# Optimization experiments

Measured on AMD Instinct MI355X. Metric: run time of the kernel, lower is better.

The kernel has to match this reference:

```python
import jax, jax.numpy as jnp
import numpy as np

T, B, NC, NM, H = 256, 2048, 3, 125, 256  # time, batch, classes, measures, hidden
IN = NC + NM


def setup_inputs() -> dict:
    key = jax.random.key(0)
    ks = jax.random.split(key, 12)
    seq = jax.random.normal(ks[0], (T, B, IN), jnp.float32)
    nan_mask = jax.random.uniform(ks[1], (T, B, IN)) < 0.1
    nan_mask = nan_mask.at[0].set(False)  # first step must be observed
    seq = jnp.where(nan_mask, jnp.nan, seq)
    s = 1.0 / np.sqrt(H)
    u = lambda k, shp: jax.random.uniform(k, shp, jnp.float32, -s, s)
    return {
        "pair_seq": seq,
        "W_ih": u(ks[2], (4 * H, IN)),
        "W_hh": u(ks[3], (4 * H, H)),
        "b_ih": u(ks[4], (4 * H,)),
        "b_hh": u(ks[5], (4 * H,)),
        "W_cat": u(ks[6], (NC, H)),
        "b_cat": u(ks[7], (NC,)),
        "W_val": u(ks[8], (NM, H)),
        "b_val": u(ks[9], (NM,)),
    }


def reference(pair_seq, W_ih, W_hh, b_ih, b_hh, W_cat, b_cat, W_val, b_val):
    cat_seq = pair_seq[:, :, :NC]
    val_seq = pair_seq[:, :, NC:]
    bsz = pair_seq.shape[1]
    h0 = jnp.zeros((bsz, H), pair_seq.dtype)
    c0 = jnp.zeros((bsz, H), pair_seq.dtype)
    # eval mode: dropout masks are all-ones, so they are identity multiplies

    def lstm_cell(x, h, c):
        gates = x @ W_ih.T + b_ih + h @ W_hh.T + b_hh  # [B, 4H]
        i, f, g, o = jnp.split(gates, 4, axis=-1)
        c2 = jax.nn.sigmoid(f) * c + jax.nn.sigmoid(i) * jnp.tanh(g)
        h2 = jax.nn.sigmoid(o) * jnp.tanh(c2)
        return h2, c2

    def step(carry, nxt):
        h, c, i_cat, i_val = carry
        cat_next, val_next = nxt
        x = jnp.concatenate([i_cat, i_val], axis=-1)
        h, c = lstm_cell(x, h, c)
        o_cat = jax.nn.softmax(h @ W_cat.T + b_cat, axis=-1)
        o_val = h @ W_val.T + b_val + i_val
        # impute NaNs in the next timestep with (detached) predictions
        i_cat2 = jnp.where(jnp.isnan(cat_next), jax.lax.stop_gradient(o_cat), cat_next)
        i_val2 = jnp.where(jnp.isnan(val_next), jax.lax.stop_gradient(o_val), val_next)
        return (h, c, i_cat2, i_val2), (o_cat, o_val)

    init = (h0, c0, cat_seq[0], val_seq[0])
    _, (out_cat, out_val) = jax.lax.scan(step, init, (cat_seq[1:], val_seq[1:]))
    return jnp.concatenate([out_cat, out_val], axis=2)  # [T-1, B, NC+NM]
```

## Files before the change

### kernel.cpp

```cpp
#include <hip/hip_runtime.h>
#include <hip/hip_bf16.h>

constexpr int TSTEPS = 255;
constexpr int XROW   = 392;

typedef __attribute__((ext_vector_type(8))) short short8;
typedef __attribute__((ext_vector_type(4))) float f32x4;
typedef __attribute__((ext_vector_type(16))) float f32x16;
typedef __attribute__((ext_vector_type(4))) int i32x4;
typedef __attribute__((ext_vector_type(2))) unsigned int u32x2;

__device__ __forceinline__ unsigned short f2bf(float f) {
    __hip_bfloat16 h = __float2bfloat16(f);
    return *reinterpret_cast<unsigned short*>(&h);
}
__device__ __forceinline__ float bf2f(unsigned short u) {
    __hip_bfloat16 h;
    *reinterpret_cast<unsigned short*>(&h) = u;
    return __bfloat162float(h);
}
__device__ __forceinline__ float sigf(float x) {
    return __builtin_amdgcn_rcpf(1.f + __expf(-x));
}
__device__ __forceinline__ float tanh_fast(float x) {
    x = fminf(fmaxf(x, -15.f), 15.f);
    float e = __expf(-2.f * x);
    return (1.f - e) * __builtin_amdgcn_rcpf(1.f + e);
}

__device__ __forceinline__ i32x4 load_coh16(const void* p) {
    i32x4 r;
    asm volatile("global_load_dwordx4 %0, %1, off sc0 sc1" : "=v"(r) : "v"(p) : "memory");
    return r;
}
__device__ __forceinline__ void store_coh16(void* p, i32x4 v) {
    asm volatile("global_store_dwordx4 %0, %1, off sc0 sc1" :: "v"(p), "v"(v) : "memory");
}

__device__ __forceinline__ void groupbar(unsigned int* cnt, unsigned int tgt, int tid) {
    asm volatile("s_waitcnt vmcnt(0)" ::: "memory");
    __syncthreads();
    if (tid == 0) {
        __hip_atomic_fetch_add(cnt, 1u, __ATOMIC_RELAXED, __HIP_MEMORY_SCOPE_AGENT);
        while (__hip_atomic_load(cnt, __ATOMIC_RELAXED, __HIP_MEMORY_SCOPE_AGENT) < tgt)
            __builtin_amdgcn_s_sleep(1);
    }
    __syncthreads();
}

__global__ void prep_kernel(const float* __restrict__ Wih, const float* __restrict__ Whh,
                            const float* __restrict__ bih, const float* __restrict__ bhh,
                            const float* __restrict__ Wcat, const float* __restrict__ bcat,
                            const float* __restrict__ Wval, const float* __restrict__ bval,
                            unsigned short* __restrict__ Wg, unsigned short* __restrict__ Wo,
                            float* __restrict__ bg, float* __restrict__ bo,
                            unsigned int* __restrict__ flags) {
    int idx = blockIdx.x * 256 + threadIdx.x;
    if (idx < 393216) {
        int j   = idx & 7;
        int l   = (idx >> 3) & 63;
        int t24 = idx >> 9;
        int kt  = t24 % 24;
        int u   = t24 / 24;
        int gm = u & 3, ss = u >> 2;
        int pm = l & 31;
        int n  = (pm & 3) * 256 + ss * 32 + gm * 8 + (pm >> 2);
        int k  = kt * 16 + (l >> 5) * 8 + j;
        float v = (k < 128) ? Wih[n * 128 + k] : Whh[n * 256 + (k - 128)];
        Wg[idx] = f2bf(v);
    } else if (idx < 425984) {
        int i2 = idx - 393216;
        int j = i2 & 7, ll = (i2 >> 3) & 63, kt = (i2 >> 9) & 15, om = i2 >> 13;
        int n = om * 32 + (ll & 31);
        int k = kt * 16 + (ll >> 5) * 8 + j;
        float v = (n < 3) ? Wcat[n * 256 + k] : Wval[(n - 3) * 256 + k];
        Wo[i2] = f2bf(v);
    } else if (idx < 427008) {
        int i3 = idx - 425984;
        bg[i3] = bih[i3] + bhh[i3];
    } else if (idx < 427136) {
        int i4 = idx - 427008;
        bo[i4] = (i4 < 3) ? bcat[i4] : bval[i4 - 3];
    } else if (idx < 428160) {
        flags[idx - 427136] = 0u;
    }
}

__global__ __launch_bounds__(512, 2) void rnn_kernel(
    const float* __restrict__ seq,
    const unsigned short* __restrict__ Wg, const unsigned short* __restrict__ Wo,
    const float* __restrict__ bg, const float* __restrict__ bo,
    unsigned short* __restrict__ hb, unsigned int* __restrict__ flags,
    float* __restrict__ out) {

    __shared__ __align__(16) unsigned short xh[64][XROW];
    __shared__ __align__(16) float bgl[128];
    __shared__ __align__(16) float obl[128];
    extern __shared__ char lds_pad[];
    (void)lds_pad;

    const int tid = threadIdx.x;
    const int wv  = tid >> 6, l = tid & 63;
    const int c   = l & 31, lh = l >> 5;
    const int s   = blockIdx.x >> 5;
    const int r   = blockIdx.x & 31;
    const int row0 = r * 64;
    const int hm  = wv >> 1;
    const int bn  = wv & 1;
    const int R   = bn * 32 + c;

    unsigned int* cnt = flags + r * 16;

    short8 wga[24], woa[16];
    {
        const short8* WgV = reinterpret_cast<const short8*>(Wg);
        const short8* WoV = reinterpret_cast<const short8*>(Wo);
#pragma unroll
        for (int kt = 0; kt < 24; ++kt) wga[kt] = WgV[(size_t)(((s * 4 + hm) * 24 + kt) * 64) + l];
#pragma unroll
        for (int kt = 0; kt < 16; ++kt) woa[kt] = WoV[(size_t)((hm * 16 + kt) * 64) + l];
    }

    if (tid < 128) {
        int gm_ = tid >> 5, lh_ = (tid >> 4) & 1, i_ = tid & 15;
        int pm = (i_ & 3) + 8 * (i_ >> 2) + 4 * lh_;
        bgl[tid] = bg[(pm & 3) * 256 + s * 32 + gm_ * 8 + (pm >> 2)];
        obl[tid] = bo[gm_ * 32 + 8 * (i_ >> 2) + 4 * lh_ + (i_ & 3)];
    }

#pragma unroll
    for (int i = 0; i < 4; ++i) {
        int ch = i * 512 + tid;
        int row = ch >> 5, c4 = ch & 31;
        f32x4 v = *reinterpret_cast<const f32x4*>(seq + (size_t)(row0 + row) * 128 + c4 * 4);
        unsigned short* p = &xh[row][c4 * 4];
        p[0] = f2bf(v[0]); p[1] = f2bf(v[1]); p[2] = f2bf(v[2]); p[3] = f2bf(v[3]);
    }
    {
        short8 z = {0, 0, 0, 0, 0, 0, 0, 0};
#pragma unroll
        for (int i = 0; i < 4; ++i) {
            int ch = i * 512 + tid;
            int row = ch >> 5, k8 = ch & 31;
            *reinterpret_cast<short8*>(&xh[row][128 + k8 * 8]) = z;
        }
    }

    unsigned int xv[8];
    {
        const float* sp0 = seq + (size_t)(row0 + R) * 128 + hm * 32 + 4 * lh;
#pragma unroll
        for (int g = 0; g < 4; ++g) {
            f32x4 v = *reinterpret_cast<const f32x4*>(sp0 + 8 * g);
            xv[2 * g]     = (unsigned int)f2bf(v[0]) | ((unsigned int)f2bf(v[1]) << 16);
            xv[2 * g + 1] = (unsigned int)f2bf(v[2]) | ((unsigned int)f2bf(v[3]) << 16);
        }
    }

    float cst[4] = {0.f, 0.f, 0.f, 0.f};
    const float* bgp = &bgl[(hm * 2 + lh) * 16];
    const float* obp = &obl[(hm * 2 + lh) * 16];
    const unsigned short* xrow = &xh[R][0];

    __syncthreads();

    for (int t = 0; t < TSTEPS; ++t) {
        f32x4 sq[4];
        if (t < TSTEPS - 1) {
            const float* sp = seq + ((size_t)(t + 1) * 2048 + row0 + R) * 128 + hm * 32 + 4 * lh;
#pragma unroll
            for (int g = 0; g < 4; ++g) sq[g] = *reinterpret_cast<const f32x4*>(sp + 8 * g);
        }

        f32x16 acc;
#pragma unroll
        for (int i = 0; i < 16; ++i) acc[i] = bgp[i];
#pragma unroll
        for (int kt = 0; kt < 24; ++kt) {
            short8 b = *reinterpret_cast<const short8*>(xrow + kt * 16 + lh * 8);
            acc = __builtin_amdgcn_mfma_f32_32x32x16_bf16(wga[kt], b, acc, 0, 0, 0);
        }

        float hn[4];
#pragma unroll
        for (int g = 0; g < 4; ++g) {
            float cn = sigf(acc[4 * g + 1]) * cst[g] + sigf(acc[4 * g]) * tanh_fast(acc[4 * g + 2]);
            hn[g] = sigf(acc[4 * g + 3]) * tanh_fast(cn);
            cst[g] = cn;
        }
        {
            i32x4 hw;
#pragma unroll
            for (int g = 0; g < 4; ++g) {
                float other = __shfl_xor(hn[g], 32);
                unsigned short lo = f2bf(lh ? other : hn[g]);
                unsigned short hi = f2bf(lh ? hn[g] : other);
                hw[g] = (int)((unsigned int)lo | ((unsigned int)hi << 16));
            }
            if (lh == 0) {
                char* hp = (char*)hb + (size_t)(t & 1) * 1048576 + (size_t)r * 32768
                         + (size_t)R * 512 + s * 64 + hm * 16;
                store_coh16(hp, hw);
            }
        }

        groupbar(cnt, 8u * (t + 1), tid);

        {
            const unsigned short* hsrc = hb + (size_t)(t & 1) * 524288 + (size_t)r * 16384;
            i32x4 hv[4];
#pragma unroll
            for (int i = 0; i < 4; ++i) {
                int ch = i * 512 + tid;
                hv[i] = load_coh16(hsrc + (size_t)((ch >> 5) * 256 + (ch & 31) * 8));
            }
            asm volatile("s_waitcnt vmcnt(0)" ::: "memory");
            __builtin_amdgcn_sched_barrier(0);
#pragma unroll
            for (int i = 0; i < 4; ++i) {
                int ch = i * 512 + tid;
                *reinterpret_cast<i32x4*>(&xh[ch >> 5][128 + (ch & 31) * 8]) = hv[i];
            }
        }
        __syncthreads();

        f32x16 acc2;
#pragma unroll
        for (int i = 0; i < 16; ++i) acc2[i] = obp[i];
#pragma unroll
        for (int kt = 0; kt < 16; ++kt) {
            short8 b = *reinterpret_cast<const short8*>(xrow + 128 + kt * 16 + lh * 8);
            acc2 = __builtin_amdgcn_mfma_f32_32x32x16_bf16(woa[kt], b, acc2, 0, 0, 0);
        }

        float vv[16];
#pragma unroll
        for (int g = 0; g < 4; ++g) {
#pragma unroll
            for (int j = 0; j < 4; ++j) {
                int i = 4 * g + j;
                float v = acc2[i];
                unsigned short x16 = (unsigned short)(xv[2 * g + (j >> 1)] >> ((j & 1) * 16));
                bool isCat = (g == 0) && (j < 3) && ((hm | lh) == 0);
                if (!isCat) v += bf2f(x16);
                vv[i] = v;
            }
        }
        if ((hm | lh) == 0) {
            float mx = fmaxf(fmaxf(vv[0], vv[1]), vv[2]);
            float e0 = __expf(vv[0] - mx), e1 = __expf(vv[1] - mx), e2 = __expf(vv[2] - mx);
            float rs = __builtin_amdgcn_rcpf(e0 + e1 + e2);
            vv[0] = e0 * rs; vv[1] = e1 * rs; vv[2] = e2 * rs;
        }

        if (hm == (s >> 1)) {
            int gp = (s & 1) * 2;
            size_t ob0 = ((size_t)t * 2048 + row0 + R) * 128 + hm * 32 + 4 * lh;
            f32x4 o0 = {vv[4 * gp], vv[4 * gp + 1], vv[4 * gp + 2], vv[4 * gp + 3]};
            f32x4 o1 = {vv[4 * gp + 4], vv[4 * gp + 5], vv[4 * gp + 6], vv[4 * gp + 7]};
            *reinterpret_cast<f32x4*>(out + ob0 + 8 * gp) = o0;
            *reinterpret_cast<f32x4*>(out + ob0 + 8 * gp + 8) = o1;
        }
        if (t < TSTEPS - 1) {
#pragma unroll
            for (int g = 0; g < 4; ++g) {
                unsigned int w0 = 0, w1 = 0;
#pragma unroll
                for (int j = 0; j < 4; ++j) {
                    unsigned short s16 = f2bf(sq[g][j]);
                    bool nan = (s16 & 0x7fff) > 0x7f80;
                    unsigned short nv = nan ? f2bf(vv[4 * g + j]) : s16;
                    if (j < 2) w0 |= (unsigned int)nv << (16 * j);
                    else       w1 |= (unsigned int)nv << (16 * (j - 2));
                }
                xv[2 * g] = w0; xv[2 * g + 1] = w1;
                u32x2 wp = {w0, w1};
                *reinterpret_cast<u32x2*>(&xh[R][hm * 32 + 8 * g + 4 * lh]) = wp;
            }
        }
        __syncthreads();
    }
}

extern "C" void kernel_launch(void* const* d_in, const int* in_sizes, int n_in,
                              void* d_out, int out_size, void* d_ws, size_t ws_size,
                              hipStream_t stream) {
    const float* seq  = (const float*)d_in[0];
    const float* Wih  = (const float*)d_in[1];
    const float* Whh  = (const float*)d_in[2];
    const float* bih  = (const float*)d_in[3];
    const float* bhh  = (const float*)d_in[4];
    const float* Wcat = (const float*)d_in[5];
    const float* bcat = (const float*)d_in[6];
    const float* Wval = (const float*)d_in[7];
    const float* bval = (const float*)d_in[8];

    char* ws = (char*)d_ws;
    unsigned short* Wg    = (unsigned short*)(ws);
    unsigned short* Wo    = (unsigned short*)(ws + 786432);
    float*          bgp   = (float*)(ws + 851968);
    float*          bop   = (float*)(ws + 856064);
    unsigned int*   flags = (unsigned int*)(ws + 856576);
    unsigned short* hbuf  = (unsigned short*)(ws + 860672);

    prep_kernel<<<1673, 256, 0, stream>>>(Wih, Whh, bih, bhh, Wcat, bcat, Wval, bval,
                                          Wg, Wo, bgp, bop, flags);
    rnn_kernel<<<256, 512, 32768, stream>>>(seq, Wg, Wo, bgp, bop, hbuf, flags, (float*)d_out);
}
```

Baseline: 1.123 ms.

## Specialize waves into gate and output roles with ping-pong batch halves

Splits each block's eight waves into four gate waves and four output waves, and splits the block's 64 batch rows into two halves processed in alternating slots. In each slot, gate waves compute the LSTM step for one half while output waves wait for the other half's h, load it, compute predictions and impute the next input. The block-wide group barrier is replaced by per-half arrival counters that only the consuming waves spin on. The gate and output MFMA chains are split into two independent accumulators, and s_setprio is raised around them. The goal is to hide cross-block h exchange latency behind matrix work. The cost is more synchronisation points per step and only half the waves doing MFMA in any slot.

New measurement: 1.378 ms. 22.7% more time.

```diff
diff --git a/kernel.cpp b/kernel.cpp
--- a/kernel.cpp
+++ b/kernel.cpp
@@ -35,17 +35,6 @@
 }
 __device__ __forceinline__ void store_coh16(void* p, i32x4 v) {
     asm volatile("global_store_dwordx4 %0, %1, off sc0 sc1" :: "v"(p), "v"(v) : "memory");
-}
-
-__device__ __forceinline__ void groupbar(unsigned int* cnt, unsigned int tgt, int tid) {
-    asm volatile("s_waitcnt vmcnt(0)" ::: "memory");
-    __syncthreads();
-    if (tid == 0) {
-        __hip_atomic_fetch_add(cnt, 1u, __ATOMIC_RELAXED, __HIP_MEMORY_SCOPE_AGENT);
-        while (__hip_atomic_load(cnt, __ATOMIC_RELAXED, __HIP_MEMORY_SCOPE_AGENT) < tgt)
-            __builtin_amdgcn_s_sleep(1);
-    }
-    __syncthreads();
 }
 
 __global__ void prep_kernel(const float* __restrict__ Wih, const float* __restrict__ Whh,
@@ -86,6 +75,133 @@
     }
 }
 
+#define SLOT(PA, TG, TO, CSTA, XVB) do {                                            \
+    constexpr int PB_ = (PA) ^ 1;                                                   \
+    const int tg_ = (TG), to_ = (TO);                                               \
+    const bool gact = isGW && (tg_ < TSTEPS);                                       \
+    const bool oact = (!isGW) && (to_ >= 0);                                        \
+    f32x16 acc, accB;                                                               \
+    f32x4 sq[4];                                                                    \
+              \
+    if (gact) {                                                                     \
+        const unsigned short* xrow = &xh[(PA) * 32 + c][0];                         \
+        _Pragma("unroll") for (int i = 0; i < 16; ++i) { acc[i] = breg[i]; accB[i] = 0.f; } \
+        __builtin_amdgcn_s_setprio(1);                                              \
+        _Pragma("unroll") for (int kt = 0; kt < 24; kt += 2) {                      \
+            short8 b0 = *reinterpret_cast<const short8*>(xrow + kt * 16 + lh * 8);  \
+            short8 b1 = *reinterpret_cast<const short8*>(xrow + (kt + 1) * 16 + lh * 8); \
+            acc  = __builtin_amdgcn_mfma_f32_32x32x16_bf16(wreg[kt], b0, acc, 0, 0, 0); \
+            accB = __builtin_amdgcn_mfma_f32_32x32x16_bf16(wreg[kt + 1], b1, accB, 0, 0, 0); \
+        }                                                                           \
+        __builtin_amdgcn_s_setprio(0);                                              \
+        _Pragma("unroll") for (int i = 0; i < 16; ++i) acc[i] += accB[i];           \
+    } else if (oact) {                                                              \
+        if (to_ + 1 < TSTEPS) {                                                     \
+            const float* sp = seq + ((size_t)(to_ + 1) * 2048 + row0 + PB_ * 32 + c) * 128 \
+                            + hm * 32 + 4 * lh;                                     \
+            _Pragma("unroll") for (int g = 0; g < 4; ++g)                           \
+                sq[g] = *reinterpret_cast<const f32x4*>(sp + 8 * g);                \
+        }                                                                           \
+        unsigned int tgt = 32u * (unsigned)(to_ + 1);                               \
+        while (__hip_atomic_load(cntP[PB_], __ATOMIC_RELAXED, __HIP_MEMORY_SCOPE_AGENT) < tgt) \
+            __builtin_amdgcn_s_sleep(1);                                            \
+        asm volatile("" ::: "memory");                                              \
+        {                                                                           \
+            const unsigned short* hsrc = hb + (size_t)(to_ & 1) * 524288 + (size_t)r * 16384; \
+            int tid2 = tid & 255;                                                   \
+            i32x4 hv[4];                                                            \
+            _Pragma("unroll") for (int i2 = 0; i2 < 4; ++i2) {                      \
+                int ch = i2 * 256 + tid2;                                           \
+                hv[i2] = load_coh16(hsrc + (size_t)((PB_ * 32 + (ch >> 5)) * 256 + (ch & 31) * 8)); \
+            }                                                                       \
+            asm volatile("s_waitcnt vmcnt(0)" ::: "memory");                        \
+            __builtin_amdgcn_sched_barrier(0);                                      \
+            _Pragma("unroll") for (int i2 = 0; i2 < 4; ++i2) {                      \
+                int ch = i2 * 256 + tid2;                                           \
+                *reinterpret_cast<i32x4*>(&xh[PB_ * 32 + (ch >> 5)][128 + (ch & 31) * 8]) = hv[i2]; \
+            }                                                                       \
+        }                                                                           \
+    }                                                                               \
+    __syncthreads();                \
+       \
+    if (gact) {                                                                     \
+        float hn[4];                                                                \
+        _Pragma("unroll") for (int g = 0; g < 4; ++g) {                             \
+            float cn = sigf(acc[4 * g + 1]) * CSTA[g]                               \
+                     + sigf(acc[4 * g + 0]) * tanh_fast(acc[4 * g + 2]);            \
+            hn[g] = sigf(acc[4 * g + 3]) * tanh_fast(cn);                           \
+            CSTA[g] = cn;                                                           \
+        }                                                                           \
+        i32x4 hw;                                                                   \
+        _Pragma("unroll") for (int g = 0; g < 4; ++g) {                             \
+            float other = __shfl_xor(hn[g], 32);                                    \
+            unsigned short lo = f2bf(lh ? other : hn[g]);                           \
+            unsigned short hi = f2bf(lh ? hn[g] : other);                           \
+            hw[g] = (int)((unsigned)lo | ((unsigned)hi << 16));                     \
+        }                                                                           \
+        if (lh == 0) {                                                              \
+            char* hp = (char*)hb + (size_t)(tg_ & 1) * 1048576 + (size_t)r * 32768  \
+                     + (size_t)((PA) * 32 + c) * 512 + s * 64 + hm * 16;            \
+            store_coh16(hp, hw);                                                    \
+        }                                                                           \
+        asm volatile("s_waitcnt vmcnt(0)" ::: "memory");                            \
+        if (l == 0)                                                                 \
+            __hip_atomic_fetch_add(cntP[PA], 1u, __ATOMIC_RELAXED, __HIP_MEMORY_SCOPE_AGENT); \
+    } else if (oact) {                                                              \
+        const unsigned short* xrow = &xh[PB_ * 32 + c][0];                          \
+        _Pragma("unroll") for (int i = 0; i < 16; ++i) { acc[i] = breg[i]; accB[i] = 0.f; } \
+        __builtin_amdgcn_s_setprio(1);                                              \
+        _Pragma("unroll") for (int kt = 0; kt < 16; kt += 2) {                      \
+            short8 b0 = *reinterpret_cast<const short8*>(xrow + 128 + kt * 16 + lh * 8); \
+            short8 b1 = *reinterpret_cast<const short8*>(xrow + 128 + (kt + 1) * 16 + lh * 8); \
+            acc  = __builtin_amdgcn_mfma_f32_32x32x16_bf16(wreg[kt], b0, acc, 0, 0, 0); \
+            accB = __builtin_amdgcn_mfma_f32_32x32x16_bf16(wreg[kt + 1], b1, accB, 0, 0, 0); \
+        }                                                                           \
+        __builtin_amdgcn_s_setprio(0);                                              \
+        float vv[16];                                                               \
+        _Pragma("unroll") for (int g = 0; g < 4; ++g) {                             \
+            _Pragma("unroll") for (int j = 0; j < 4; ++j) {                         \
+                int i = 4 * g + j;                                                  \
+                float v = acc[i] + accB[i];                                         \
+                unsigned short x16 = (unsigned short)(XVB[2 * g + (j >> 1)] >> ((j & 1) * 16)); \
+                bool isCat = (g == 0) && (j < 3) && hm0lh0;                         \
+                if (!isCat) v += bf2f(x16);                                         \
+                vv[i] = v;                                                          \
+            }                                                                       \
+        }                                                                           \
+        if (hm0lh0) {                                                               \
+            float mx = fmaxf(fmaxf(vv[0], vv[1]), vv[2]);                           \
+            float e0 = __expf(vv[0] - mx), e1 = __expf(vv[1] - mx), e2 = __expf(vv[2] - mx); \
+            float rs = __builtin_amdgcn_rcpf(e0 + e1 + e2);                         \
+            vv[0] = e0 * rs; vv[1] = e1 * rs; vv[2] = e2 * rs;                      \
+        }                                                                           \
+        if (hm == (s >> 1)) {                                                       \
+            int gp = (s & 1) * 2;                                                   \
+            size_t ob0 = ((size_t)to_ * 2048 + row0 + PB_ * 32 + c) * 128 + hm * 32 + 4 * lh; \
+            f32x4 o0 = {vv[4 * gp], vv[4 * gp + 1], vv[4 * gp + 2], vv[4 * gp + 3]}; \
+            f32x4 o1 = {vv[4 * gp + 4], vv[4 * gp + 5], vv[4 * gp + 6], vv[4 * gp + 7]}; \
+            *reinterpret_cast<f32x4*>(out + ob0 + 8 * gp) = o0;                     \
+            *reinterpret_cast<f32x4*>(out + ob0 + 8 * gp + 8) = o1;                 \
+        }                                                                           \
+        if (to_ < TSTEPS - 1) {                                                     \
+            _Pragma("unroll") for (int g = 0; g < 4; ++g) {                         \
+                unsigned int w0 = 0, w1 = 0;                                        \
+                _Pragma("unroll") for (int j = 0; j < 4; ++j) {                     \
+                    float sqv = sq[g][j];                                           \
+                    float xf = (sqv != sqv) ? vv[4 * g + j] : sqv;                  \
+                    unsigned short nv = f2bf(xf);                                   \
+                    if (j < 2) w0 |= (unsigned)nv << (16 * j);                      \
+                    else       w1 |= (unsigned)nv << (16 * (j - 2));                \
+                }                                                                   \
+                XVB[2 * g] = w0; XVB[2 * g + 1] = w1;                               \
+                u32x2 wp = {w0, w1};                                                \
+                *reinterpret_cast<u32x2*>(&xh[PB_ * 32 + c][hm * 32 + 8 * g + 4 * lh]) = wp; \
+            }                                                                       \
+        }                                                                           \
+    }                                                                               \
+    __syncthreads();                                                  \
+} while (0)
+
 __global__ __launch_bounds__(512, 2) void rnn_kernel(
     const float* __restrict__ seq,
     const unsigned short* __restrict__ Wg, const unsigned short* __restrict__ Wo,
@@ -105,20 +221,23 @@
     const int s   = blockIdx.x >> 5;
     const int r   = blockIdx.x & 31;
     const int row0 = r * 64;
-    const int hm  = wv >> 1;
-    const int bn  = wv & 1;
-    const int R   = bn * 32 + c;
-
-    unsigned int* cnt = flags + r * 16;
-
-    short8 wga[24], woa[16];
-    {
+    const bool isGW = wv < 4;
+    const int hm  = wv & 3;
+    const bool hm0lh0 = (hm == 0) && (lh == 0);
+
+    unsigned int* cntP[2] = {flags + r * 32, flags + r * 32 + 16};
+
+    short8 wreg[24];
+    if (isGW) {
         const short8* WgV = reinterpret_cast<const short8*>(Wg);
+#pragma unroll
+        for (int kt = 0; kt < 24; ++kt) wreg[kt] = WgV[(size_t)(((s * 4 + hm) * 24 + kt) * 64) + l];
+    } else {
         const short8* WoV = reinterpret_cast<const short8*>(Wo);
 #pragma unroll
-        for (int kt = 0; kt < 24; ++kt) wga[kt] = WgV[(size_t)(((s * 4 + hm) * 24 + kt) * 64) + l];
-#pragma unroll
-        for (int kt = 0; kt < 16; ++kt) woa[kt] = WoV[(size_t)((hm * 16 + kt) * 64) + l];
+        for (int kt = 0; kt < 16; ++kt) wreg[kt] = WoV[(size_t)((hm * 16 + kt) * 64) + l];
+#pragma unroll
+        for (int kt = 16; kt < 24; ++kt) wreg[kt] = wreg[0];
     }
 
     if (tid < 128) {
@@ -141,145 +260,43 @@
 #pragma unroll
         for (int i = 0; i < 4; ++i) {
             int ch = i * 512 + tid;
-            int row = ch >> 5, k8 = ch & 31;
-            *reinterpret_cast<short8*>(&xh[row][128 + k8 * 8]) = z;
+            *reinterpret_cast<short8*>(&xh[ch >> 5][128 + (ch & 31) * 8]) = z;
         }
     }
 
-    unsigned int xv[8];
-    {
-        const float* sp0 = seq + (size_t)(row0 + R) * 128 + hm * 32 + 4 * lh;
+    unsigned int xv0[8], xv1[8];
+    if (!isGW) {
+        const float* sp0 = seq + (size_t)(row0 + c) * 128 + hm * 32 + 4 * lh;
 #pragma unroll
         for (int g = 0; g < 4; ++g) {
             f32x4 v = *reinterpret_cast<const f32x4*>(sp0 + 8 * g);
-            xv[2 * g]     = (unsigned int)f2bf(v[0]) | ((unsigned int)f2bf(v[1]) << 16);
-            xv[2 * g + 1] = (unsigned int)f2bf(v[2]) | ((unsigned int)f2bf(v[3]) << 16);
+            xv0[2 * g]     = (unsigned)f2bf(v[0]) | ((unsigned)f2bf(v[1]) << 16);
+            xv0[2 * g + 1] = (unsigned)f2bf(v[2]) | ((unsigned)f2bf(v[3]) << 16);
         }
-    }
-
-    float cst[4] = {0.f, 0.f, 0.f, 0.f};
-    const float* bgp = &bgl[(hm * 2 + lh) * 16];
-    const float* obp = &obl[(hm * 2 + lh) * 16];
-    const unsigned short* xrow = &xh[R][0];
+        const float* sp1 = seq + (size_t)(row0 + 32 + c) * 128 + hm * 32 + 4 * lh;
+#pragma unroll
+        for (int g = 0; g < 4; ++g) {
+            f32x4 v = *reinterpret_cast<const f32x4*>(sp1 + 8 * g);
+            xv1[2 * g]     = (unsigned)f2bf(v[0]) | ((unsigned)f2bf(v[1]) << 16);
+            xv1[2 * g + 1] = (unsigned)f2bf(v[2]) | ((unsigned)f2bf(v[3]) << 16);
+        }
+    }
+
+    float cst0[4] = {0.f, 0.f, 0.f, 0.f};
+    float cst1[4] = {0.f, 0.f, 0.f, 0.f};
 
     __syncthreads();
 
-    for (int t = 0; t < TSTEPS; ++t) {
-        f32x4 sq[4];
-        if (t < TSTEPS - 1) {
-            const float* sp = seq + ((size_t)(t + 1) * 2048 + row0 + R) * 128 + hm * 32 + 4 * lh;
-#pragma unroll
-            for (int g = 0; g < 4; ++g) sq[g] = *reinterpret_cast<const f32x4*>(sp + 8 * g);
-        }
-
-        f32x16 acc;
-#pragma unroll
-        for (int i = 0; i < 16; ++i) acc[i] = bgp[i];
-#pragma unroll
-        for (int kt = 0; kt < 24; ++kt) {
-            short8 b = *reinterpret_cast<const short8*>(xrow + kt * 16 + lh * 8);
-            acc = __builtin_amdgcn_mfma_f32_32x32x16_bf16(wga[kt], b, acc, 0, 0, 0);
-        }
-
-        float hn[4];
-#pragma unroll
-        for (int g = 0; g < 4; ++g) {
-            float cn = sigf(acc[4 * g + 1]) * cst[g] + sigf(acc[4 * g]) * tanh_fast(acc[4 * g + 2]);
-            hn[g] = sigf(acc[4 * g + 3]) * tanh_fast(cn);
-            cst[g] = cn;
-        }
-        {
-            i32x4 hw;
-#pragma unroll
-            for (int g = 0; g < 4; ++g) {
-                float other = __shfl_xor(hn[g], 32);
-                unsigned short lo = f2bf(lh ? other : hn[g]);
-                unsigned short hi = f2bf(lh ? hn[g] : other);
-                hw[g] = (int)((unsigned int)lo | ((unsigned int)hi << 16));
-            }
-            if (lh == 0) {
-                char* hp = (char*)hb + (size_t)(t & 1) * 1048576 + (size_t)r * 32768
-                         + (size_t)R * 512 + s * 64 + hm * 16;
-                store_coh16(hp, hw);
-            }
-        }
-
-        groupbar(cnt, 8u * (t + 1), tid);
-
-        {
-            const unsigned short* hsrc = hb + (size_t)(t & 1) * 524288 + (size_t)r * 16384;
-            i32x4 hv[4];
-#pragma unroll
-            for (int i = 0; i < 4; ++i) {
-                int ch = i * 512 + tid;
-                hv[i] = load_coh16(hsrc + (size_t)((ch >> 5) * 256 + (ch & 31) * 8));
-            }
-            asm volatile("s_waitcnt vmcnt(0)" ::: "memory");
-            __builtin_amdgcn_sched_barrier(0);
-#pragma unroll
-            for (int i = 0; i < 4; ++i) {
-                int ch = i * 512 + tid;
-                *reinterpret_cast<i32x4*>(&xh[ch >> 5][128 + (ch & 31) * 8]) = hv[i];
-            }
-        }
-        __syncthreads();
-
-        f32x16 acc2;
-#pragma unroll
-        for (int i = 0; i < 16; ++i) acc2[i] = obp[i];
-#pragma unroll
-        for (int kt = 0; kt < 16; ++kt) {
-            short8 b = *reinterpret_cast<const short8*>(xrow + 128 + kt * 16 + lh * 8);
-            acc2 = __builtin_amdgcn_mfma_f32_32x32x16_bf16(woa[kt], b, acc2, 0, 0, 0);
-        }
-
-        float vv[16];
-#pragma unroll
-        for (int g = 0; g < 4; ++g) {
-#pragma unroll
-            for (int j = 0; j < 4; ++j) {
-                int i = 4 * g + j;
-                float v = acc2[i];
-                unsigned short x16 = (unsigned short)(xv[2 * g + (j >> 1)] >> ((j & 1) * 16));
-                bool isCat = (g == 0) && (j < 3) && ((hm | lh) == 0);
-                if (!isCat) v += bf2f(x16);
-                vv[i] = v;
-            }
-        }
-        if ((hm | lh) == 0) {
-            float mx = fmaxf(fmaxf(vv[0], vv[1]), vv[2]);
-            float e0 = __expf(vv[0] - mx), e1 = __expf(vv[1] - mx), e2 = __expf(vv[2] - mx);
-            float rs = __builtin_amdgcn_rcpf(e0 + e1 + e2);
-            vv[0] = e0 * rs; vv[1] = e1 * rs; vv[2] = e2 * rs;
-        }
-
-        if (hm == (s >> 1)) {
-            int gp = (s & 1) * 2;
-            size_t ob0 = ((size_t)t * 2048 + row0 + R) * 128 + hm * 32 + 4 * lh;
-            f32x4 o0 = {vv[4 * gp], vv[4 * gp + 1], vv[4 * gp + 2], vv[4 * gp + 3]};
-            f32x4 o1 = {vv[4 * gp + 4], vv[4 * gp + 5], vv[4 * gp + 6], vv[4 * gp + 7]};
-            *reinterpret_cast<f32x4*>(out + ob0 + 8 * gp) = o0;
-            *reinterpret_cast<f32x4*>(out + ob0 + 8 * gp + 8) = o1;
-        }
-        if (t < TSTEPS - 1) {
-#pragma unroll
-            for (int g = 0; g < 4; ++g) {
-                unsigned int w0 = 0, w1 = 0;
-#pragma unroll
-                for (int j = 0; j < 4; ++j) {
-                    unsigned short s16 = f2bf(sq[g][j]);
-                    bool nan = (s16 & 0x7fff) > 0x7f80;
-                    unsigned short nv = nan ? f2bf(vv[4 * g + j]) : s16;
-                    if (j < 2) w0 |= (unsigned int)nv << (16 * j);
-                    else       w1 |= (unsigned int)nv << (16 * (j - 2));
-                }
-                xv[2 * g] = w0; xv[2 * g + 1] = w1;
-                u32x2 wp = {w0, w1};
-                *reinterpret_cast<u32x2*>(&xh[R][hm * 32 + 8 * g + 4 * lh]) = wp;
-            }
-        }
-        __syncthreads();
-    }
+    float breg[16];
+#pragma unroll
+    for (int i = 0; i < 16; ++i)
+        breg[i] = isGW ? bgl[(hm * 2 + lh) * 16 + i] : obl[(hm * 2 + lh) * 16 + i];
+
+    for (int tt = 0; tt < TSTEPS; ++tt) {
+        SLOT(0, tt, tt - 1, cst0, xv1);
+        SLOT(1, tt, tt,     cst1, xv0);
+    }
+    SLOT(0, TSTEPS, TSTEPS - 1, cst0, xv1);
 }
 
 extern "C" void kernel_launch(void* const* d_in, const int* in_sizes, int n_in,
```

## Split batch into 32-row blocks with 4 waves and dual MFMA accumulators

Applied to the files above, without the earlier changes.

Changes the decomposition from 256 blocks of 512 threads (64 batch rows) to 512 blocks of 256 threads (32 batch rows), with each wave covering one hidden slice. The gate and output matmuls now alternate between two independent accumulators to break the MFMA dependency chain, and run at raised wave priority. The NaN imputation test now checks the fp32 value before conversion. The extra dynamic LDS padding controls occupancy. Doubling the number of groups syncing through the global barrier may add synchronisation cost, and the summed split accumulators slightly change rounding order.

After: 1.493 ms. 33.0% more time.

```diff
diff --git a/kernel.cpp b/kernel.cpp
--- a/kernel.cpp
+++ b/kernel.cpp
@@ -86,14 +86,14 @@
     }
 }
 
-__global__ __launch_bounds__(512, 2) void rnn_kernel(
+__global__ __launch_bounds__(256, 2) void rnn_kernel(
     const float* __restrict__ seq,
     const unsigned short* __restrict__ Wg, const unsigned short* __restrict__ Wo,
     const float* __restrict__ bg, const float* __restrict__ bo,
     unsigned short* __restrict__ hb, unsigned int* __restrict__ flags,
     float* __restrict__ out) {
 
-    __shared__ __align__(16) unsigned short xh[64][XROW];
+    __shared__ __align__(16) unsigned short xh[32][XROW];
     __shared__ __align__(16) float bgl[128];
     __shared__ __align__(16) float obl[128];
     extern __shared__ char lds_pad[];
@@ -102,12 +102,11 @@
     const int tid = threadIdx.x;
     const int wv  = tid >> 6, l = tid & 63;
     const int c   = l & 31, lh = l >> 5;
-    const int s   = blockIdx.x >> 5;
-    const int r   = blockIdx.x & 31;
-    const int row0 = r * 64;
-    const int hm  = wv >> 1;
-    const int bn  = wv & 1;
-    const int R   = bn * 32 + c;
+    const int s   = blockIdx.x & 7;
+    const int r   = blockIdx.x >> 3;
+    const int row0 = r * 32;
+    const int hm  = wv;
+    const bool hm0lh0 = (hm == 0) && (lh == 0);
 
     unsigned int* cnt = flags + r * 16;
 
@@ -130,7 +129,7 @@
 
 #pragma unroll
     for (int i = 0; i < 4; ++i) {
-        int ch = i * 512 + tid;
+        int ch = i * 256 + tid;
         int row = ch >> 5, c4 = ch & 31;
         f32x4 v = *reinterpret_cast<const f32x4*>(seq + (size_t)(row0 + row) * 128 + c4 * 4);
         unsigned short* p = &xh[row][c4 * 4];
@@ -140,46 +139,51 @@
         short8 z = {0, 0, 0, 0, 0, 0, 0, 0};
 #pragma unroll
         for (int i = 0; i < 4; ++i) {
-            int ch = i * 512 + tid;
-            int row = ch >> 5, k8 = ch & 31;
-            *reinterpret_cast<short8*>(&xh[row][128 + k8 * 8]) = z;
+            int ch = i * 256 + tid;
+            *reinterpret_cast<short8*>(&xh[ch >> 5][128 + (ch & 31) * 8]) = z;
         }
     }
 
     unsigned int xv[8];
     {
-        const float* sp0 = seq + (size_t)(row0 + R) * 128 + hm * 32 + 4 * lh;
+        const float* sp0 = seq + (size_t)(row0 + c) * 128 + hm * 32 + 4 * lh;
 #pragma unroll
         for (int g = 0; g < 4; ++g) {
             f32x4 v = *reinterpret_cast<const f32x4*>(sp0 + 8 * g);
-            xv[2 * g]     = (unsigned int)f2bf(v[0]) | ((unsigned int)f2bf(v[1]) << 16);
-            xv[2 * g + 1] = (unsigned int)f2bf(v[2]) | ((unsigned int)f2bf(v[3]) << 16);
+            xv[2 * g]     = (unsigned)f2bf(v[0]) | ((unsigned)f2bf(v[1]) << 16);
+            xv[2 * g + 1] = (unsigned)f2bf(v[2]) | ((unsigned)f2bf(v[3]) << 16);
         }
     }
 
     float cst[4] = {0.f, 0.f, 0.f, 0.f};
     const float* bgp = &bgl[(hm * 2 + lh) * 16];
     const float* obp = &obl[(hm * 2 + lh) * 16];
-    const unsigned short* xrow = &xh[R][0];
+    const unsigned short* xrow = &xh[c][0];
 
     __syncthreads();
 
     for (int t = 0; t < TSTEPS; ++t) {
         f32x4 sq[4];
         if (t < TSTEPS - 1) {
-            const float* sp = seq + ((size_t)(t + 1) * 2048 + row0 + R) * 128 + hm * 32 + 4 * lh;
+            const float* sp = seq + ((size_t)(t + 1) * 2048 + row0 + c) * 128 + hm * 32 + 4 * lh;
 #pragma unroll
             for (int g = 0; g < 4; ++g) sq[g] = *reinterpret_cast<const f32x4*>(sp + 8 * g);
         }
 
-        f32x16 acc;
-#pragma unroll
-        for (int i = 0; i < 16; ++i) acc[i] = bgp[i];
-#pragma unroll
-        for (int kt = 0; kt < 24; ++kt) {
-            short8 b = *reinterpret_cast<const short8*>(xrow + kt * 16 + lh * 8);
-            acc = __builtin_amdgcn_mfma_f32_32x32x16_bf16(wga[kt], b, acc, 0, 0, 0);
-        }
+        f32x16 acc, accB;
+#pragma unroll
+        for (int i = 0; i < 16; ++i) { acc[i] = bgp[i]; accB[i] = 0.f; }
+        __builtin_amdgcn_s_setprio(1);
+#pragma unroll
+        for (int kt = 0; kt < 24; kt += 2) {
+            short8 b0 = *reinterpret_cast<const short8*>(xrow + kt * 16 + lh * 8);
+            short8 b1 = *reinterpret_cast<const short8*>(xrow + (kt + 1) * 16 + lh * 8);
+            acc  = __builtin_amdgcn_mfma_f32_32x32x16_bf16(wga[kt], b0, acc, 0, 0, 0);
+            accB = __builtin_amdgcn_mfma_f32_32x32x16_bf16(wga[kt + 1], b1, accB, 0, 0, 0);
+        }
+        __builtin_amdgcn_s_setprio(0);
+#pragma unroll
+        for (int i = 0; i < 16; ++i) acc[i] += accB[i];
 
         float hn[4];
 #pragma unroll
@@ -195,11 +199,11 @@
                 float other = __shfl_xor(hn[g], 32);
                 unsigned short lo = f2bf(lh ? other : hn[g]);
                 unsigned short hi = f2bf(lh ? hn[g] : other);
-                hw[g] = (int)((unsigned int)lo | ((unsigned int)hi << 16));
+                hw[g] = (int)((unsigned)lo | ((unsigned)hi << 16));
             }
             if (lh == 0) {
-                char* hp = (char*)hb + (size_t)(t & 1) * 1048576 + (size_t)r * 32768
-                         + (size_t)R * 512 + s * 64 + hm * 16;
+                char* hp = (char*)hb + (size_t)(t & 1) * 1048576 + (size_t)r * 16384
+                         + (size_t)c * 512 + s * 64 + hm * 16;
                 store_coh16(hp, hw);
             }
         }
@@ -207,31 +211,35 @@
         groupbar(cnt, 8u * (t + 1), tid);
 
         {
-            const unsigned short* hsrc = hb + (size_t)(t & 1) * 524288 + (size_t)r * 16384;
+            const unsigned short* hsrc = hb + (size_t)(t & 1) * 524288 + (size_t)r * 8192;
             i32x4 hv[4];
 #pragma unroll
             for (int i = 0; i < 4; ++i) {
-                int ch = i * 512 + tid;
+                int ch = i * 256 + tid;
                 hv[i] = load_coh16(hsrc + (size_t)((ch >> 5) * 256 + (ch & 31) * 8));
             }
             asm volatile("s_waitcnt vmcnt(0)" ::: "memory");
             __builtin_amdgcn_sched_barrier(0);
 #pragma unroll
             for (int i = 0; i < 4; ++i) {
-                int ch = i * 512 + tid;
+                int ch = i * 256 + tid;
                 *reinterpret_cast<i32x4*>(&xh[ch >> 5][128 + (ch & 31) * 8]) = hv[i];
             }
         }
         __syncthreads();
 
-        f32x16 acc2;
-#pragma unroll
-        for (int i = 0; i < 16; ++i) acc2[i] = obp[i];
-#pragma unroll
-        for (int kt = 0; kt < 16; ++kt) {
-            short8 b = *reinterpret_cast<const short8*>(xrow + 128 + kt * 16 + lh * 8);
-            acc2 = __builtin_amdgcn_mfma_f32_32x32x16_bf16(woa[kt], b, acc2, 0, 0, 0);
-        }
+        f32x16 acc2, acc2B;
+#pragma unroll
+        for (int i = 0; i < 16; ++i) { acc2[i] = obp[i]; acc2B[i] = 0.f; }
+        __builtin_amdgcn_s_setprio(1);
+#pragma unroll
+        for (int kt = 0; kt < 16; kt += 2) {
+            short8 b0 = *reinterpret_cast<const short8*>(xrow + 128 + kt * 16 + lh * 8);
+            short8 b1 = *reinterpret_cast<const short8*>(xrow + 128 + (kt + 1) * 16 + lh * 8);
+            acc2  = __builtin_amdgcn_mfma_f32_32x32x16_bf16(woa[kt], b0, acc2, 0, 0, 0);
+            acc2B = __builtin_amdgcn_mfma_f32_32x32x16_bf16(woa[kt + 1], b1, acc2B, 0, 0, 0);
+        }
+        __builtin_amdgcn_s_setprio(0);
 
         float vv[16];
 #pragma unroll
@@ -239,14 +247,14 @@
 #pragma unroll
             for (int j = 0; j < 4; ++j) {
                 int i = 4 * g + j;
-                float v = acc2[i];
+                float v = acc2[i] + acc2B[i];
                 unsigned short x16 = (unsigned short)(xv[2 * g + (j >> 1)] >> ((j & 1) * 16));
-                bool isCat = (g == 0) && (j < 3) && ((hm | lh) == 0);
+                bool isCat = (g == 0) && (j < 3) && hm0lh0;
                 if (!isCat) v += bf2f(x16);
                 vv[i] = v;
             }
         }
-        if ((hm | lh) == 0) {
+        if (hm0lh0) {
             float mx = fmaxf(fmaxf(vv[0], vv[1]), vv[2]);
             float e0 = __expf(vv[0] - mx), e1 = __expf(vv[1] - mx), e2 = __expf(vv[2] - mx);
             float rs = __builtin_amdgcn_rcpf(e0 + e1 + e2);
@@ -255,7 +263,7 @@
 
         if (hm == (s >> 1)) {
             int gp = (s & 1) * 2;
-            size_t ob0 = ((size_t)t * 2048 + row0 + R) * 128 + hm * 32 + 4 * lh;
+            size_t ob0 = ((size_t)t * 2048 + row0 + c) * 128 + hm * 32 + 4 * lh;
             f32x4 o0 = {vv[4 * gp], vv[4 * gp + 1], vv[4 * gp + 2], vv[4 * gp + 3]};
             f32x4 o1 = {vv[4 * gp + 4], vv[4 * gp + 5], vv[4 * gp + 6], vv[4 * gp + 7]};
             *reinterpret_cast<f32x4*>(out + ob0 + 8 * gp) = o0;
@@ -267,15 +275,15 @@
                 unsigned int w0 = 0, w1 = 0;
 #pragma unroll
                 for (int j = 0; j < 4; ++j) {
-                    unsigned short s16 = f2bf(sq[g][j]);
-                    bool nan = (s16 & 0x7fff) > 0x7f80;
-                    unsigned short nv = nan ? f2bf(vv[4 * g + j]) : s16;
-                    if (j < 2) w0 |= (unsigned int)nv << (16 * j);
-                    else       w1 |= (unsigned int)nv << (16 * (j - 2));
+                    float sqv = sq[g][j];
+                    float xf = (sqv != sqv) ? vv[4 * g + j] : sqv;
+                    unsigned short nv = f2bf(xf);
+                    if (j < 2) w0 |= (unsigned)nv << (16 * j);
+                    else       w1 |= (unsigned)nv << (16 * (j - 2));
                 }
                 xv[2 * g] = w0; xv[2 * g + 1] = w1;
                 u32x2 wp = {w0, w1};
-                *reinterpret_cast<u32x2*>(&xh[R][hm * 32 + 8 * g + 4 * lh]) = wp;
+                *reinterpret_cast<u32x2*>(&xh[c][hm * 32 + 8 * g + 4 * lh]) = wp;
             }
         }
         __syncthreads();
@@ -305,5 +313,5 @@
 
     prep_kernel<<<1673, 256, 0, stream>>>(Wih, Whh, bih, bhh, Wcat, bcat, Wval, bval,
                                           Wg, Wo, bgp, bop, flags);
-    rnn_kernel<<<256, 512, 32768, stream>>>(seq, Wg, Wo, bgp, bop, hbuf, flags, (float*)d_out);
-}
+    rnn_kernel<<<512, 256, 53248, stream>>>(seq, Wg, Wo, bgp, bop, hbuf, flags, (float*)d_out);
+}
```

## Fuse recurrent h-projection into output GEMM loop and split group barrier

Applied to the files above, without the earlier changes.

The gate GEMM is split into an input part (8 k-tiles over x) and a recurrent part (16 k-tiles over h). The recurrent part now runs in the same loop as the output projection, since both read the freshly gathered h tile. The LSTM cell update, h publish and per-wave atomic arrival move to the end of the previous iteration. The next iteration only spins on the counter, which removes the block-wide sync around the barrier and a separate pass over h. It also adds s_setprio around the MFMA loops and peels a first step. The cost is more register pressure from the second accumulator and tighter ordering assumptions on the double-buffered h.

Measured after the change: 3.962 ms. 253% more time.

```diff
diff --git a/kernel.cpp b/kernel.cpp
--- a/kernel.cpp
+++ b/kernel.cpp
@@ -35,17 +35,6 @@
 }
 __device__ __forceinline__ void store_coh16(void* p, i32x4 v) {
     asm volatile("global_store_dwordx4 %0, %1, off sc0 sc1" :: "v"(p), "v"(v) : "memory");
-}
-
-__device__ __forceinline__ void groupbar(unsigned int* cnt, unsigned int tgt, int tid) {
-    asm volatile("s_waitcnt vmcnt(0)" ::: "memory");
-    __syncthreads();
-    if (tid == 0) {
-        __hip_atomic_fetch_add(cnt, 1u, __ATOMIC_RELAXED, __HIP_MEMORY_SCOPE_AGENT);
-        while (__hip_atomic_load(cnt, __ATOMIC_RELAXED, __HIP_MEMORY_SCOPE_AGENT) < tgt)
-            __builtin_amdgcn_s_sleep(1);
-    }
-    __syncthreads();
 }
 
 __global__ void prep_kernel(const float* __restrict__ Wih, const float* __restrict__ Whh,
@@ -108,6 +97,7 @@
     const int hm  = wv >> 1;
     const int bn  = wv & 1;
     const int R   = bn * 32 + c;
+    const bool hm0lh0 = (hm == 0) && (lh == 0);
 
     unsigned int* cnt = flags + r * 16;
 
@@ -136,15 +126,6 @@
         unsigned short* p = &xh[row][c4 * 4];
         p[0] = f2bf(v[0]); p[1] = f2bf(v[1]); p[2] = f2bf(v[2]); p[3] = f2bf(v[3]);
     }
-    {
-        short8 z = {0, 0, 0, 0, 0, 0, 0, 0};
-#pragma unroll
-        for (int i = 0; i < 4; ++i) {
-            int ch = i * 512 + tid;
-            int row = ch >> 5, k8 = ch & 31;
-            *reinterpret_cast<short8*>(&xh[row][128 + k8 * 8]) = z;
-        }
-    }
 
     unsigned int xv[8];
     {
@@ -152,8 +133,8 @@
 #pragma unroll
         for (int g = 0; g < 4; ++g) {
             f32x4 v = *reinterpret_cast<const f32x4*>(sp0 + 8 * g);
-            xv[2 * g]     = (unsigned int)f2bf(v[0]) | ((unsigned int)f2bf(v[1]) << 16);
-            xv[2 * g + 1] = (unsigned int)f2bf(v[2]) | ((unsigned int)f2bf(v[3]) << 16);
+            xv[2 * g]     = (unsigned)f2bf(v[0]) | ((unsigned)f2bf(v[1]) << 16);
+            xv[2 * g + 1] = (unsigned)f2bf(v[2]) | ((unsigned)f2bf(v[3]) << 16);
         }
     }
 
@@ -164,7 +145,50 @@
 
     __syncthreads();
 
+#define LSTM_TAIL(ACC, GEN) do {                                                     \
+        float hn_[4];                                                                \
+        _Pragma("unroll") for (int g = 0; g < 4; ++g) {                              \
+            float cn = sigf((ACC)[4 * g + 1]) * cst[g]                               \
+                     + sigf((ACC)[4 * g]) * tanh_fast((ACC)[4 * g + 2]);             \
+            hn_[g] = sigf((ACC)[4 * g + 3]) * tanh_fast(cn);                         \
+            cst[g] = cn;                                                             \
+        }                                                                            \
+        i32x4 hw_;                                                                   \
+        _Pragma("unroll") for (int g = 0; g < 4; ++g) {                              \
+            float other = __shfl_xor(hn_[g], 32);                                    \
+            unsigned short lo = f2bf(lh ? other : hn_[g]);                           \
+            unsigned short hi = f2bf(lh ? hn_[g] : other);                           \
+            hw_[g] = (int)((unsigned)lo | ((unsigned)hi << 16));                     \
+        }                                                                            \
+        if (lh == 0) {                                                               \
+            char* hp = (char*)hb + (size_t)((GEN) & 1) * 1048576 + (size_t)r * 32768 \
+                     + (size_t)R * 512 + s * 64 + hm * 16;                           \
+            store_coh16(hp, hw_);                                                    \
+        }                                                                            \
+        asm volatile("s_waitcnt vmcnt(0)" ::: "memory");                             \
+        if (l == 0)                                                                  \
+            __hip_atomic_fetch_add(cnt, 1u, __ATOMIC_RELAXED, __HIP_MEMORY_SCOPE_AGENT); \
+    } while (0)
+
+    {
+        f32x16 acc;
+#pragma unroll
+        for (int i = 0; i < 16; ++i) acc[i] = bgp[i];
+#pragma unroll
+        for (int kt = 0; kt < 8; ++kt) {
+            short8 b = *reinterpret_cast<const short8*>(xrow + kt * 16 + lh * 8);
+            acc = __builtin_amdgcn_mfma_f32_32x32x16_bf16(wga[kt], b, acc, 0, 0, 0);
+        }
+        LSTM_TAIL(acc, 1);
+    }
+
     for (int t = 0; t < TSTEPS; ++t) {
+        {
+            unsigned int tgt = 64u * (unsigned)(t + 1);
+            while (__hip_atomic_load(cnt, __ATOMIC_RELAXED, __HIP_MEMORY_SCOPE_AGENT) < tgt)
+                __builtin_amdgcn_s_sleep(1);
+        }
+
         f32x4 sq[4];
         if (t < TSTEPS - 1) {
             const float* sp = seq + ((size_t)(t + 1) * 2048 + row0 + R) * 128 + hm * 32 + 4 * lh;
@@ -172,42 +196,8 @@
             for (int g = 0; g < 4; ++g) sq[g] = *reinterpret_cast<const f32x4*>(sp + 8 * g);
         }
 
-        f32x16 acc;
-#pragma unroll
-        for (int i = 0; i < 16; ++i) acc[i] = bgp[i];
-#pragma unroll
-        for (int kt = 0; kt < 24; ++kt) {
-            short8 b = *reinterpret_cast<const short8*>(xrow + kt * 16 + lh * 8);
-            acc = __builtin_amdgcn_mfma_f32_32x32x16_bf16(wga[kt], b, acc, 0, 0, 0);
-        }
-
-        float hn[4];
-#pragma unroll
-        for (int g = 0; g < 4; ++g) {
-            float cn = sigf(acc[4 * g + 1]) * cst[g] + sigf(acc[4 * g]) * tanh_fast(acc[4 * g + 2]);
-            hn[g] = sigf(acc[4 * g + 3]) * tanh_fast(cn);
-            cst[g] = cn;
-        }
         {
-            i32x4 hw;
-#pragma unroll
-            for (int g = 0; g < 4; ++g) {
-                float other = __shfl_xor(hn[g], 32);
-                unsigned short lo = f2bf(lh ? other : hn[g]);
-                unsigned short hi = f2bf(lh ? hn[g] : other);
-                hw[g] = (int)((unsigned int)lo | ((unsigned int)hi << 16));
-            }
-            if (lh == 0) {
-                char* hp = (char*)hb + (size_t)(t & 1) * 1048576 + (size_t)r * 32768
-                         + (size_t)R * 512 + s * 64 + hm * 16;
-                store_coh16(hp, hw);
-            }
-        }
-
-        groupbar(cnt, 8u * (t + 1), tid);
-
-        {
-            const unsigned short* hsrc = hb + (size_t)(t & 1) * 524288 + (size_t)r * 16384;
+            const unsigned short* hsrc = hb + (size_t)((t + 1) & 1) * 524288 + (size_t)r * 16384;
             i32x4 hv[4];
 #pragma unroll
             for (int i = 0; i < 4; ++i) {
@@ -224,14 +214,17 @@
         }
         __syncthreads();
 
-        f32x16 acc2;
-#pragma unroll
-        for (int i = 0; i < 16; ++i) acc2[i] = obp[i];
+        f32x16 acc_o, acc_gh;
+#pragma unroll
+        for (int i = 0; i < 16; ++i) { acc_o[i] = obp[i]; acc_gh[i] = 0.f; }
+        __builtin_amdgcn_s_setprio(1);
 #pragma unroll
         for (int kt = 0; kt < 16; ++kt) {
             short8 b = *reinterpret_cast<const short8*>(xrow + 128 + kt * 16 + lh * 8);
-            acc2 = __builtin_amdgcn_mfma_f32_32x32x16_bf16(woa[kt], b, acc2, 0, 0, 0);
-        }
+            acc_o  = __builtin_amdgcn_mfma_f32_32x32x16_bf16(woa[kt], b, acc_o, 0, 0, 0);
+            acc_gh = __builtin_amdgcn_mfma_f32_32x32x16_bf16(wga[8 + kt], b, acc_gh, 0, 0, 0);
+        }
+        __builtin_amdgcn_s_setprio(0);
 
         float vv[16];
 #pragma unroll
@@ -239,14 +232,14 @@
 #pragma unroll
             for (int j = 0; j < 4; ++j) {
                 int i = 4 * g + j;
-                float v = acc2[i];
+                float v = acc_o[i];
                 unsigned short x16 = (unsigned short)(xv[2 * g + (j >> 1)] >> ((j & 1) * 16));
-                bool isCat = (g == 0) && (j < 3) && ((hm | lh) == 0);
+                bool isCat = (g == 0) && (j < 3) && hm0lh0;
                 if (!isCat) v += bf2f(x16);
                 vv[i] = v;
             }
         }
-        if ((hm | lh) == 0) {
+        if (hm0lh0) {
             float mx = fmaxf(fmaxf(vv[0], vv[1]), vv[2]);
             float e0 = __expf(vv[0] - mx), e1 = __expf(vv[1] - mx), e2 = __expf(vv[2] - mx);
             float rs = __builtin_amdgcn_rcpf(e0 + e1 + e2);
@@ -270,8 +263,8 @@
                     unsigned short s16 = f2bf(sq[g][j]);
                     bool nan = (s16 & 0x7fff) > 0x7f80;
                     unsigned short nv = nan ? f2bf(vv[4 * g + j]) : s16;
-                    if (j < 2) w0 |= (unsigned int)nv << (16 * j);
-                    else       w1 |= (unsigned int)nv << (16 * (j - 2));
+                    if (j < 2) w0 |= (unsigned)nv << (16 * j);
+                    else       w1 |= (unsigned)nv << (16 * (j - 2));
                 }
                 xv[2 * g] = w0; xv[2 * g + 1] = w1;
                 u32x2 wp = {w0, w1};
@@ -279,7 +272,22 @@
             }
         }
         __syncthreads();
-    }
+
+        if (t < TSTEPS - 1) {
+            f32x16 acc;
+#pragma unroll
+            for (int i = 0; i < 16; ++i) acc[i] = acc_gh[i] + bgp[i];
+            __builtin_amdgcn_s_setprio(1);
+#pragma unroll
+            for (int kt = 0; kt < 8; ++kt) {
+                short8 b = *reinterpret_cast<const short8*>(xrow + kt * 16 + lh * 8);
+                acc = __builtin_amdgcn_mfma_f32_32x32x16_bf16(wga[kt], b, acc, 0, 0, 0);
+            }
+            __builtin_amdgcn_s_setprio(0);
+            LSTM_TAIL(acc, t + 2);
+        }
+    }
+#undef LSTM_TAIL
 }
 
 extern "C" void kernel_launch(void* const* d_in, const int* in_sizes, int n_in,
```
